# Optimization experiments

Hardware: AMD Instinct MI355X
Metric: run time of the kernel (lower is better)

## Reference

```python
import jax, jax.numpy as jnp
import numpy as np


def conv1x1(x, W, b):
    # x: [B, C, H, W], W: [O, C], b: [O] -> [B, O, H, W]
    return jnp.einsum('bchw,oc->bohw', x, W) + b[None, :, None, None]


def setup_inputs() -> dict:
    key = jax.random.key(0)
    ks = jax.random.split(key, 8)
    B, C, H, W = 8, 128, 64, 64
    d = C // 8
    s = 0.05
    return {
        'x': jax.random.normal(ks[0], (B, C, H, W), jnp.float32),
        'Wq': jax.random.normal(ks[1], (d, C), jnp.float32) * s,
        'bq': jax.random.normal(ks[2], (d,), jnp.float32) * s,
        'Wk': jax.random.normal(ks[3], (d, C), jnp.float32) * s,
        'bk': jax.random.normal(ks[4], (d,), jnp.float32) * s,
        'Wv': jax.random.normal(ks[5], (C, C), jnp.float32) * s,
        'bv': jax.random.normal(ks[6], (C,), jnp.float32) * s,
        'gamma': jax.random.normal(ks[7], (1,), jnp.float32),
    }


def reference(x, Wq, bq, Wk, bk, Wv, bv, gamma):
    B, C, H, W = x.shape
    N = H * W
    q = conv1x1(x, Wq, bq).reshape(B, -1, N)      # [B, d, N]
    k = conv1x1(x, Wk, bk).reshape(B, -1, N)      # [B, d, N]
    v = conv1x1(x, Wv, bv).reshape(B, C, N)       # [B, C, N]
    # energy[b, i, j] = q_i . k_j  (no scaling, as in original)
    energy = jnp.einsum('bdi,bdj->bij', q, k)     # [B, N, N]
    attn = jax.nn.softmax(energy, axis=-1)
    # out[b, c, i] = sum_j v[b, c, j] * attn[b, i, j]
    out = jnp.einsum('bcj,bij->bci', v, attn).reshape(B, C, H, W)
    return gamma[0] * out + x
```

## Files before the change

kernel.cpp:

```cpp
#include <hip/hip_runtime.h>

#define BATCH 8
#define CCH   128
#define DQK   16
#define HW    4096
#define LOG2E 1.44269504088896340736f
#define KTS   24
#define WTS   136
#define WGRAN 2816

typedef __attribute__((ext_vector_type(8))) short bf16x8;
typedef __attribute__((ext_vector_type(4))) float f32x4;

__device__ __forceinline__ unsigned cvt_pk_bf16(float lo, float hi) {
    unsigned r;
    asm("v_cvt_pk_bf16_f32 %0, %1, %2" : "=v"(r) : "v"(lo), "v"(hi));
    return r;
}

__device__ __forceinline__ void glds16(const void* gsrc, const void* lds) {
    auto* g = (const __attribute__((address_space(1))) unsigned int*)(unsigned long long)(uintptr_t)gsrc;
    auto* s = (__attribute__((address_space(3))) unsigned int*)(unsigned int)(uintptr_t)lds;
    __builtin_amdgcn_global_load_lds(g, s, 16, 0, 0);
}

__global__ __launch_bounds__(256) void prep_kernel(
    const float* __restrict__ Wq, const float* __restrict__ Wk,
    const float* __restrict__ Wv, ushort* __restrict__ Wpad)
{
    const int idx = blockIdx.x * 256 + threadIdx.x;
    if (idx >= 160 * (WTS / 2)) return;
    const int row = idx / (WTS / 2);
    const int c0  = (idx % (WTS / 2)) * 2;
    unsigned val = 0;
    if (c0 < CCH) {
        const float* src;
        float sc = 1.f;
        if (row < 16)       { src = Wq + row * CCH;        sc = LOG2E; }
        else if (row < 32)  { src = Wk + (row - 16) * CCH; }
        else                { src = Wv + (row - 32) * CCH; }
        val = cvt_pk_bf16(src[c0] * sc, src[c0 + 1] * sc);
    }
    *(unsigned*)&Wpad[row * WTS + c0] = val;
}

__global__ __launch_bounds__(256) void qkv_kernel(
    const float* __restrict__ x, const ushort* __restrict__ Wpad,
    const float* __restrict__ bq, const float* __restrict__ bk,
    const float* __restrict__ bv,
    ushort* __restrict__ qT, ushort* __restrict__ kT, ushort* __restrict__ v)
{
    const int blk = blockIdx.x;
    const int b   = blk >> 6;
    const int p0  = (blk & 63) << 6;
    const int t   = threadIdx.x;
    const int l   = t & 63;
    const int w   = t >> 6;
    const int lm  = l & 15;
    const int lg  = l >> 4;

    __shared__ __align__(16) ushort W_l[WGRAN * 8];
    __shared__ __align__(16) ushort xT_l[64 * WTS];

#pragma unroll
    for (int i = 0; i < 11; i++) {
        const int idx = t + 256 * i;
        glds16(Wpad + idx * 8, &W_l[idx * 8]);
    }

#pragma unroll
    for (int it = 0; it < 4; it++) {
        const int oc = w + 4 * it;
        float xr[8];
#pragma unroll
        for (int r = 0; r < 8; r++)
            xr[r] = x[((size_t)(b * CCH + oc * 8 + r)) * HW + p0 + l];
        unsigned u[4];
#pragma unroll
        for (int r = 0; r < 4; r++) u[r] = cvt_pk_bf16(xr[2 * r], xr[2 * r + 1]);
        *(bf16x8*)&xT_l[l * WTS + oc * 8] = *(bf16x8*)u;
    }
    __syncthreads();

    bf16x8 bfrag[4];
#pragma unroll
    for (int ks = 0; ks < 4; ks++)
        bfrag[ks] = *(const bf16x8*)&xT_l[(w * 16 + lm) * WTS + ks * 32 + lg * 8];

    f32x4 acc[10];
#pragma unroll
    for (int ot = 0; ot < 10; ot++)
#pragma unroll
        for (int r = 0; r < 4; r++) acc[ot][r] = 0.f;

#pragma unroll
    for (int ot = 0; ot < 10; ot++) {
#pragma unroll
        for (int ks = 0; ks < 4; ks++) {
            const bf16x8 afrag = *(const bf16x8*)&W_l[(ot * 16 + lm) * WTS + ks * 32 + lg * 8];
            acc[ot] = __builtin_amdgcn_mfma_f32_16x16x32_bf16(afrag, bfrag[ks], acc[ot], 0, 0, 0);
        }
    }

    const int px = p0 + w * 16 + lm;
#pragma unroll
    for (int ot = 0; ot < 10; ot++) {
        const int ob = ot * 16 + 4 * lg;
        float4 bb;
        if (ot == 0) {
            bb = *(const float4*)(bq + 4 * lg);
            bb.x *= LOG2E; bb.y *= LOG2E; bb.z *= LOG2E; bb.w *= LOG2E;
        } else if (ot == 1) {
            bb = *(const float4*)(bk + 4 * lg);
        } else {
            bb = *(const float4*)(bv + (ot - 2) * 16 + 4 * lg);
        }
        const float r0 = acc[ot][0] + bb.x, r1 = acc[ot][1] + bb.y;
        const float r2 = acc[ot][2] + bb.z, r3 = acc[ot][3] + bb.w;
        const unsigned w0 = cvt_pk_bf16(r0, r1), w1 = cvt_pk_bf16(r2, r3);
        if (ot == 0) {
            uint2 pk; pk.x = w0; pk.y = w1;
            *(uint2*)&qT[((size_t)(b * HW + px)) * DQK + ob] = pk;
        } else if (ot == 1) {
            uint2 pk; pk.x = w0; pk.y = w1;
            *(uint2*)&kT[((size_t)(b * HW + px)) * KTS + (ob - 16)] = pk;
        } else {
            const int c = ob - 32;
            v[((size_t)(b * CCH + c + 0)) * HW + px] = (ushort)(w0 & 0xffff);
            v[((size_t)(b * CCH + c + 1)) * HW + px] = (ushort)(w0 >> 16);
            v[((size_t)(b * CCH + c + 2)) * HW + px] = (ushort)(w1 & 0xffff);
            v[((size_t)(b * CCH + c + 3)) * HW + px] = (ushort)(w1 >> 16);
        }
    }
}

__global__ __launch_bounds__(256) void attn_kernel(
    const ushort* __restrict__ qT, const ushort* __restrict__ kTg,
    const ushort* __restrict__ vg, const float* __restrict__ x,
    const float* __restrict__ gamma, float* __restrict__ out)
{
    const int blk = ((blockIdx.x & 7) << 6) | (blockIdx.x >> 3);
    const int b   = blk >> 6;
    const int i0  = (blk & 63) << 6;
    const int t   = threadIdx.x;
    const int l   = t & 63;
    const int w   = t >> 6;
    const int lm  = l & 15;
    const int lg  = l >> 4;

    __shared__ __align__(16) ushort kT_l[128 * KTS];
    __shared__ __align__(16) ushort v_l [128 * 128];
    __shared__ __align__(16) ushort P_l [64 * 128];

    const ushort* kT_src0 = kTg + ((size_t)b * HW) * KTS + t * 8;
    const ushort* kT_src1 = kTg + ((size_t)b * HW) * KTS + (256 + t) * 8;
    ushort*       kT_dst0 = &kT_l[t * 8];
    ushort*       kT_dst1 = &kT_l[(256 + t) * 8];
    const ushort* v_src[8];
    ushort*       v_dst[8];
#pragma unroll
    for (int it = 0; it < 8; it++) {
        const int idx = t + 256 * it;
        const int c   = idx >> 4;
        const int gs  = (idx & 15) ^ (c & 15);
        v_src[it] = vg + ((size_t)(b * CCH + c)) * HW + gs * 8;
        v_dst[it] = &v_l[idx * 8];
    }

    bf16x8 qf;
#pragma unroll
    for (int z = 0; z < 8; z++) qf[z] = 0;
    if (lg < 2)
        qf = *(const bf16x8*)(qT + ((size_t)(b * HW + i0 + 16 * w + lm)) * DQK + lg * 8);

    f32x4 zero4;
#pragma unroll
    for (int z = 0; z < 4; z++) zero4[z] = 0.f;

    f32x4 acc[8];
#pragma unroll
    for (int ct = 0; ct < 8; ct++) acc[ct] = zero4;

    float m_i = -1e30f, l_i = 0.f;

    for (int j0 = 0; j0 < HW; j0 += 128) {
        __syncthreads();

        glds16(kT_src0 + (size_t)j0 * KTS, kT_dst0);
        if (t < 128)
            glds16(kT_src1 + (size_t)j0 * KTS, kT_dst1);
#pragma unroll
        for (int it = 0; it < 8; it++)
            glds16(v_src[it] + j0, v_dst[it]);
        __syncthreads();

        f32x4 s[8];
#pragma unroll
        for (int jt = 0; jt < 8; jt++) {
            bf16x8 kf = {};
            if (lg < 2)
                kf = *(const bf16x8*)&kT_l[(jt * 16 + lm) * KTS + lg * 8];
            s[jt] = __builtin_amdgcn_mfma_f32_16x16x32_bf16(kf, qf, zero4, 0, 0, 0);
        }

        float mx = s[0][0];
#pragma unroll
        for (int jt = 0; jt < 8; jt++)
#pragma unroll
            for (int r = 0; r < 4; r++) mx = fmaxf(mx, s[jt][r]);
        mx = fmaxf(mx, __shfl_xor(mx, 16));
        mx = fmaxf(mx, __shfl_xor(mx, 32));

        float m_new, alpha;
        if (__all(mx - m_i <= 8.f)) {
            m_new = m_i; alpha = 1.f;
        } else {
            m_new = fmaxf(m_i, mx);
            alpha = exp2f(m_i - m_new);
#pragma unroll
            for (int ct = 0; ct < 8; ct++) acc[ct] *= alpha;
        }

        float sum = 0.f;
        const int prow = (16 * w + lm) * 128;
#pragma unroll
        for (int jt = 0; jt < 8; jt++) {
            const float p0f = exp2f(s[jt][0] - m_new);
            const float p1f = exp2f(s[jt][1] - m_new);
            const float p2f = exp2f(s[jt][2] - m_new);
            const float p3f = exp2f(s[jt][3] - m_new);
            sum += (p0f + p1f) + (p2f + p3f);
            uint2 pk;
            pk.x = cvt_pk_bf16(p0f, p1f);
            pk.y = cvt_pk_bf16(p2f, p3f);
            const int g = (2 * jt + (lg >> 1)) ^ lm;
            *(uint2*)&P_l[prow + g * 8 + (lg & 1) * 4] = pk;
        }
        sum += __shfl_xor(sum, 16);
        sum += __shfl_xor(sum, 32);
        l_i = l_i * alpha + sum;
        m_i = m_new;

        __builtin_amdgcn_s_setprio(1);
#pragma unroll
        for (int ks = 0; ks < 4; ks++) {
            const int g = (4 * ks + lg) ^ lm;
            const bf16x8 pf = *(const bf16x8*)&P_l[prow + g * 8];
#pragma unroll
            for (int ct = 0; ct < 8; ct++) {
                const bf16x8 vf = *(const bf16x8*)&v_l[(ct * 16 + lm) * 128 + g * 8];
                acc[ct] = __builtin_amdgcn_mfma_f32_16x16x32_bf16(vf, pf, acc[ct], 0, 0, 0);
            }
        }
        __builtin_amdgcn_s_setprio(0);
    }

    const float linv = 1.f / l_i;
    const float gm = gamma[0];
    const int i = 16 * w + lm;
#pragma unroll
    for (int ct = 0; ct < 8; ct++) {
#pragma unroll
        for (int r = 0; r < 4; r++) {
            const int c = ct * 16 + lg * 4 + r;
            const size_t off = ((size_t)(b * CCH + c)) * HW + i0 + i;
            out[off] = gm * (acc[ct][r] * linv) + x[off];
        }
    }
}

extern "C" void kernel_launch(void* const* d_in, const int* in_sizes, int n_in,
                              void* d_out, int out_size, void* d_ws, size_t ws_size,
                              hipStream_t stream)
{
    const float* x     = (const float*)d_in[0];
    const float* Wq    = (const float*)d_in[1];
    const float* bq    = (const float*)d_in[2];
    const float* Wk    = (const float*)d_in[3];
    const float* bk    = (const float*)d_in[4];
    const float* Wv    = (const float*)d_in[5];
    const float* bv    = (const float*)d_in[6];
    const float* gamma = (const float*)d_in[7];
    float* out = (float*)d_out;

    ushort* qT   = (ushort*)d_ws;
    ushort* kT   = qT + (size_t)BATCH * HW * DQK;
    ushort* v    = kT + (size_t)BATCH * HW * KTS;
    ushort* Wpad = v  + (size_t)BATCH * CCH * HW;

    prep_kernel<<<dim3(43), dim3(256), 0, stream>>>(Wq, Wk, Wv, Wpad);
    qkv_kernel<<<dim3(BATCH * (HW / 64)), dim3(256), 0, stream>>>(
        x, Wpad, bq, bk, bv, qT, kT, v);
    attn_kernel<<<dim3(BATCH * (HW / 64)), dim3(256), 0, stream>>>(
        qT, kT, v, x, gamma, out);
}
```

Measured before the change: 173.5 us.

## Stage x via LDS DMA, coalesce v stores, read K directly from global

The qkv kernel now loads x with global_load_lds into LDS and builds the B fragments from LDS instead of gathering strided global loads. It stages the v output through an LDS transpose buffer so each row is written to global memory as coalesced 16-byte chunks. The attention kernel drops the K tile from LDS and reads K fragments directly from global memory. This moves the barrier so the QK^T and softmax work can overlap the in-flight v DMA. The risk is higher global-load latency on the K path and more LDS use in qkv, which could lower occupancy.

```diff
diff --git a/kernel.cpp b/kernel.cpp
--- a/kernel.cpp
+++ b/kernel.cpp
@@ -8,6 +8,7 @@
 #define KTS   24
 #define WTS   136
 #define WGRAN 2816
+#define VTP   72
 
 typedef __attribute__((ext_vector_type(8))) short bf16x8;
 typedef __attribute__((ext_vector_type(4))) float f32x4;
@@ -59,33 +60,34 @@
     const int lm  = l & 15;
     const int lg  = l >> 4;
 
+    __shared__ __align__(16) float  x_l[CCH * 64];
     __shared__ __align__(16) ushort W_l[WGRAN * 8];
-    __shared__ __align__(16) ushort xT_l[64 * WTS];
-
+
+#pragma unroll
+    for (int i = 0; i < 8; i++) {
+        const int idx = t + 256 * i;
+        glds16(x + (size_t)b * CCH * HW + (size_t)(idx >> 4) * HW + p0 + (idx & 15) * 4,
+               &x_l[idx * 4]);
+    }
 #pragma unroll
     for (int i = 0; i < 11; i++) {
         const int idx = t + 256 * i;
         glds16(Wpad + idx * 8, &W_l[idx * 8]);
     }
-
-#pragma unroll
-    for (int it = 0; it < 4; it++) {
-        const int oc = w + 4 * it;
+    __syncthreads();
+
+    bf16x8 bfrag[4];
+#pragma unroll
+    for (int ks = 0; ks < 4; ks++) {
         float xr[8];
 #pragma unroll
         for (int r = 0; r < 8; r++)
-            xr[r] = x[((size_t)(b * CCH + oc * 8 + r)) * HW + p0 + l];
+            xr[r] = x_l[(ks * 32 + lg * 8 + r) * 64 + 16 * w + lm];
         unsigned u[4];
 #pragma unroll
         for (int r = 0; r < 4; r++) u[r] = cvt_pk_bf16(xr[2 * r], xr[2 * r + 1]);
-        *(bf16x8*)&xT_l[l * WTS + oc * 8] = *(bf16x8*)u;
-    }
-    __syncthreads();
-
-    bf16x8 bfrag[4];
-#pragma unroll
-    for (int ks = 0; ks < 4; ks++)
-        bfrag[ks] = *(const bf16x8*)&xT_l[(w * 16 + lm) * WTS + ks * 32 + lg * 8];
+        bfrag[ks] = *(bf16x8*)u;
+    }
 
     f32x4 acc[10];
 #pragma unroll
@@ -102,35 +104,43 @@
         }
     }
 
-    const int px = p0 + w * 16 + lm;
-#pragma unroll
-    for (int ot = 0; ot < 10; ot++) {
-        const int ob = ot * 16 + 4 * lg;
-        float4 bb;
-        if (ot == 0) {
-            bb = *(const float4*)(bq + 4 * lg);
-            bb.x *= LOG2E; bb.y *= LOG2E; bb.z *= LOG2E; bb.w *= LOG2E;
-        } else if (ot == 1) {
-            bb = *(const float4*)(bk + 4 * lg);
-        } else {
-            bb = *(const float4*)(bv + (ot - 2) * 16 + 4 * lg);
-        }
-        const float r0 = acc[ot][0] + bb.x, r1 = acc[ot][1] + bb.y;
-        const float r2 = acc[ot][2] + bb.z, r3 = acc[ot][3] + bb.w;
-        const unsigned w0 = cvt_pk_bf16(r0, r1), w1 = cvt_pk_bf16(r2, r3);
-        if (ot == 0) {
-            uint2 pk; pk.x = w0; pk.y = w1;
-            *(uint2*)&qT[((size_t)(b * HW + px)) * DQK + ob] = pk;
-        } else if (ot == 1) {
-            uint2 pk; pk.x = w0; pk.y = w1;
-            *(uint2*)&kT[((size_t)(b * HW + px)) * KTS + (ob - 16)] = pk;
-        } else {
-            const int c = ob - 32;
-            v[((size_t)(b * CCH + c + 0)) * HW + px] = (ushort)(w0 & 0xffff);
-            v[((size_t)(b * CCH + c + 1)) * HW + px] = (ushort)(w0 >> 16);
-            v[((size_t)(b * CCH + c + 2)) * HW + px] = (ushort)(w1 & 0xffff);
-            v[((size_t)(b * CCH + c + 3)) * HW + px] = (ushort)(w1 >> 16);
-        }
+    const int px_loc = 16 * w + lm;
+    const int px     = p0 + px_loc;
+    {
+        float4 bb = *(const float4*)(bq + 4 * lg);
+        uint2 pk;
+        pk.x = cvt_pk_bf16(acc[0][0] + bb.x * LOG2E, acc[0][1] + bb.y * LOG2E);
+        pk.y = cvt_pk_bf16(acc[0][2] + bb.z * LOG2E, acc[0][3] + bb.w * LOG2E);
+        *(uint2*)&qT[((size_t)(b * HW + px)) * DQK + 4 * lg] = pk;
+    }
+    {
+        float4 bb = *(const float4*)(bk + 4 * lg);
+        uint2 pk;
+        pk.x = cvt_pk_bf16(acc[1][0] + bb.x, acc[1][1] + bb.y);
+        pk.y = cvt_pk_bf16(acc[1][2] + bb.z, acc[1][3] + bb.w);
+        *(uint2*)&kT[((size_t)(b * HW + px)) * KTS + 4 * lg] = pk;
+    }
+
+    __syncthreads();
+    ushort* vt = (ushort*)x_l;
+#pragma unroll
+    for (int ot = 2; ot < 10; ot++) {
+        const int cv = (ot - 2) * 16 + 4 * lg;
+        const float4 bb = *(const float4*)(bv + cv);
+        const unsigned w0 = cvt_pk_bf16(acc[ot][0] + bb.x, acc[ot][1] + bb.y);
+        const unsigned w1 = cvt_pk_bf16(acc[ot][2] + bb.z, acc[ot][3] + bb.w);
+        vt[(cv + 0) * VTP + px_loc] = (ushort)(w0 & 0xffff);
+        vt[(cv + 1) * VTP + px_loc] = (ushort)(w0 >> 16);
+        vt[(cv + 2) * VTP + px_loc] = (ushort)(w1 & 0xffff);
+        vt[(cv + 3) * VTP + px_loc] = (ushort)(w1 >> 16);
+    }
+    __syncthreads();
+#pragma unroll
+    for (int i = 0; i < 4; i++) {
+        const int u = t + 256 * i;
+        const int c = u >> 3, oct = u & 7;
+        const bf16x8 vv = *(const bf16x8*)&vt[c * VTP + oct * 8];
+        *(bf16x8*)&v[((size_t)(b * CCH + c)) * HW + p0 + oct * 8] = vv;
     }
 }
 
@@ -148,14 +158,9 @@
     const int lm  = l & 15;
     const int lg  = l >> 4;
 
-    __shared__ __align__(16) ushort kT_l[128 * KTS];
-    __shared__ __align__(16) ushort v_l [128 * 128];
-    __shared__ __align__(16) ushort P_l [64 * 128];
-
-    const ushort* kT_src0 = kTg + ((size_t)b * HW) * KTS + t * 8;
-    const ushort* kT_src1 = kTg + ((size_t)b * HW) * KTS + (256 + t) * 8;
-    ushort*       kT_dst0 = &kT_l[t * 8];
-    ushort*       kT_dst1 = &kT_l[(256 + t) * 8];
+    __shared__ __align__(16) ushort v_l[128 * 128];
+    __shared__ __align__(16) ushort P_l[64 * 128];
+
     const ushort* v_src[8];
     ushort*       v_dst[8];
 #pragma unroll
@@ -186,20 +191,17 @@
     for (int j0 = 0; j0 < HW; j0 += 128) {
         __syncthreads();
 
-        glds16(kT_src0 + (size_t)j0 * KTS, kT_dst0);
-        if (t < 128)
-            glds16(kT_src1 + (size_t)j0 * KTS, kT_dst1);
 #pragma unroll
         for (int it = 0; it < 8; it++)
             glds16(v_src[it] + j0, v_dst[it]);
-        __syncthreads();
-
+
+        const ushort* kbase = kTg + ((size_t)b * HW + j0) * KTS;
         f32x4 s[8];
 #pragma unroll
         for (int jt = 0; jt < 8; jt++) {
             bf16x8 kf = {};
             if (lg < 2)
-                kf = *(const bf16x8*)&kT_l[(jt * 16 + lm) * KTS + lg * 8];
+                kf = *(const bf16x8*)(kbase + (jt * 16 + lm) * KTS + lg * 8);
             s[jt] = __builtin_amdgcn_mfma_f32_16x16x32_bf16(kf, qf, zero4, 0, 0, 0);
         }
 
@@ -240,6 +242,8 @@
         sum += __shfl_xor(sum, 32);
         l_i = l_i * alpha + sum;
         m_i = m_new;
+
+        __syncthreads();
 
         __builtin_amdgcn_s_setprio(1);
 #pragma unroll
```

Result: slower. 218.8 us (+26.1%).
